# Performance work log

Measured on AMD Instinct MI355X. Metric: run time of the kernel, lower is better.

## Reference

```python
import jax, jax.numpy as jnp
import numpy as np

B, C, H, W, Q = 4, 64, 128, 128, 30000
HID = 256
IN_DIM = C * 9 + 4  # unfolded feat + rel_coord(2) + rel_cell(2)


def setup_inputs() -> dict:
    key = jax.random.key(0)
    ks = jax.random.split(key, 14)
    inp = jax.random.normal(ks[0], (B, 1, H, W), jnp.float32)
    coord = jax.random.uniform(ks[1], (B, Q, 2), jnp.float32, -1.0, 1.0)
    cell = jnp.full((B, Q, 2), 2.0 / 256.0, jnp.float32)  # HR cell size for 256x256 target
    conv_w = jax.random.normal(ks[2], (C, 1, 3, 3), jnp.float32) * 0.3
    conv_b = jnp.zeros((C,), jnp.float32)
    def lin(k, fi, fo):
        return jax.random.normal(k, (fi, fo), jnp.float32) * (1.0 / np.sqrt(fi))
    w1 = lin(ks[3], IN_DIM, HID); b1 = jnp.zeros((HID,), jnp.float32)
    w2 = lin(ks[4], HID, HID);    b2 = jnp.zeros((HID,), jnp.float32)
    w3 = lin(ks[5], HID, HID);    b3 = jnp.zeros((HID,), jnp.float32)
    w4 = lin(ks[6], HID, HID);    b4 = jnp.zeros((HID,), jnp.float32)
    w5 = lin(ks[7], HID, 1);      b5 = jnp.zeros((1,), jnp.float32)
    return dict(inp=inp, coord=coord, cell=cell, conv_w=conv_w, conv_b=conv_b,
                w1=w1, b1=b1, w2=w2, b2=b2, w3=w3, b3=b3, w4=w4, b4=b4, w5=w5, b5=b5)


def _mlp(x, w1, b1, w2, b2, w3, b3, w4, b4, w5, b5):
    h = jax.nn.relu(x @ w1 + b1)
    h = jax.nn.relu(h @ w2 + b2)
    h = jax.nn.relu(h @ w3 + b3)
    h = jax.nn.relu(h @ w4 + b4)
    return h @ w5 + b5


def reference(inp, coord, cell, conv_w, conv_b, w1, b1, w2, b2, w3, b3, w4, b4, w5, b5):
    # encoder: conv3x3, pad 1 (NCHW)
    feat = jax.lax.conv_general_dilated(
        inp, conv_w, window_strides=(1, 1), padding=((1, 1), (1, 1)),
        dimension_numbers=("NCHW", "OIHW", "NCHW")) + conv_b[None, :, None, None]
    # feat_unfold: F.unfold(feat, 3, padding=1).view(B, C*9, H, W)
    pad = jnp.pad(feat, ((0, 0), (0, 0), (1, 1), (1, 1)))
    patches = jnp.stack([pad[:, :, kh:kh + H, kw:kw + W]
                         for kh in range(3) for kw in range(3)], axis=2)  # (B,C,9,H,W)
    featu = patches.reshape(B, C * 9, H, W)
    featu_t = featu.transpose(0, 2, 3, 1).reshape(B, H * W, C * 9)  # (B,HW,Cu)

    rx = 1.0 / H  # 2/H/2
    ry = 1.0 / W
    eps_shift = 1e-6
    Hf = jnp.float32(H); Wf = jnp.float32(W)
    rel_cell = cell * jnp.array([H, W], jnp.float32)  # same for all branches

    preds, areas = [], []
    for vx in (-1.0, 1.0):
        for vy in (-1.0, 1.0):
            c0 = jnp.clip(coord[..., 0] + vx * rx + eps_shift, -1 + 1e-6, 1 - 1e-6)
            c1 = jnp.clip(coord[..., 1] + vy * ry + eps_shift, -1 + 1e-6, 1 - 1e-6)
            # nearest grid_sample, align_corners=False (round half-to-even = nearbyint)
            i = jnp.clip(jnp.round((c0 + 1.0) * Hf / 2.0 - 0.5), 0.0, Hf - 1.0)
            j = jnp.clip(jnp.round((c1 + 1.0) * Wf / 2.0 - 0.5), 0.0, Wf - 1.0)
            # q_coord = feat_coord sampled at same nearest index (pixel centers)
            qy = -1.0 + (2.0 * i + 1.0) / Hf
            qx = -1.0 + (2.0 * j + 1.0) / Wf
            idx = (i * Wf + j).astype(jnp.int32)  # (B,Q)
            q_feat = jnp.take_along_axis(featu_t, idx[..., None], axis=1)  # (B,Q,Cu)
            rel0 = (coord[..., 0] - qy) * Hf
            rel1 = (coord[..., 1] - qx) * Wf
            x = jnp.concatenate([q_feat, rel0[..., None], rel1[..., None], rel_cell], axis=-1)
            pred = _mlp(x.reshape(B * Q, -1), w1, b1, w2, b2, w3, b3, w4, b4, w5, b5)
            preds.append(pred.reshape(B, Q, -1))
            areas.append(jnp.abs(rel0 * rel1) + 1e-9)

    tot_area = areas[0] + areas[1] + areas[2] + areas[3]
    # local_ensemble: swap diagonally-opposite areas
    areas = [areas[3], areas[2], areas[1], areas[0]]
    ret = jnp.zeros_like(preds[0])
    for pred, area in zip(preds, areas):
        ret = ret + pred * (area / tot_area)[..., None]
    return ret  # (B, Q, 1)
```

## Files before the change

### kernel.cpp

```cpp
#include <hip/hip_runtime.h>
#include <stdint.h>


typedef unsigned short u16;
typedef __attribute__((ext_vector_type(8))) short   short8;
typedef __attribute__((ext_vector_type(8))) __bf16  bf16x8;
typedef __attribute__((ext_vector_type(4))) float   f32x4;

__device__ __forceinline__ float bf2f(u16 u) {
  union { uint32_t i; float f; } v; v.i = ((uint32_t)u) << 16; return v.f;
}
__device__ __forceinline__ u16 f2bf(float f) {
  union { float f; uint32_t i; } v; v.f = f;
  return (u16)((v.i + 0x7FFFu + ((v.i >> 16) & 1u)) >> 16);
}
__device__ __forceinline__ u16 bfbits(float f) {
  union { __bf16 h; u16 u; } c; c.h = (__bf16)f; return c.u;
}

__global__ void prep_weights(const float* __restrict__ w1, const float* __restrict__ w2,
                             const float* __restrict__ w3, const float* __restrict__ w4,
                             u16* __restrict__ w1pt, u16* __restrict__ w2t,
                             u16* __restrict__ w3t, u16* __restrict__ w4t) {
  int tid = blockIdx.x * 256 + threadIdx.x;
  const int N1 = 256 * 576;
  if (tid < N1) {
    int o = tid / 576, kk = tid - o * 576;
    int t = kk >> 6, c = kk & 63;
    w1pt[tid] = f2bf(w1[(c * 9 + t) * 256 + o]);
  } else {
    int u = tid - N1;
    if (u < 3 * 65536) {
      int layer = u >> 16, r = u & 65535;
      int o = r >> 8, k = r & 255;
      const float* src = (layer == 0) ? w2 : (layer == 1) ? w3 : w4;
      u16* dst = (layer == 0) ? w2t : (layer == 1) ? w3t : w4t;
      dst[o * 256 + k] = f2bf(src[k * 256 + o]);
    }
  }
}

__global__ void conv1_kernel(const float* __restrict__ inp, const float* __restrict__ cw,
                             const float* __restrict__ cb, u16* __restrict__ feat) {
  int tid = blockIdx.x * 256 + threadIdx.x;
  int c = tid & 63;
  int x = (tid >> 6) & 127;
  int y = (tid >> 13) & 127;
  int b = tid >> 20;
  const float* ip = inp + b * 16384;
  float s = cb[c];
  #pragma unroll
  for (int kh = 0; kh < 3; ++kh) {
    int iy = y + kh - 1;
    if (iy < 0 || iy > 127) continue;
    #pragma unroll
    for (int kw = 0; kw < 3; ++kw) {
      int ix = x + kw - 1;
      if (ix < 0 || ix > 127) continue;
      s += ip[iy * 128 + ix] * cw[c * 9 + kh * 3 + kw];
    }
  }
  feat[tid] = f2bf(s);
}

__global__ __launch_bounds__(256) void layer1_kernel(const u16* __restrict__ feat,
                                                     const u16* __restrict__ w1pt,
                                                     const float* __restrict__ b1,
                                                     u16* __restrict__ h1pre) {
  __shared__ short Al[64 * 40];
  __shared__ short Wl[256 * 40];

  int tid = threadIdx.x;
  int lane = tid & 63, wave = tid >> 6;
  int bid = blockIdx.x;
  int b = bid >> 8, rem = bid & 255;
  int y = rem >> 1, x0 = (rem & 1) << 6;

  f32x4 acc[4][4];
  #pragma unroll
  for (int i = 0; i < 4; ++i)
    #pragma unroll
    for (int j = 0; j < 4; ++j) acc[i][j] = (f32x4){0.f, 0.f, 0.f, 0.f};

  int apx = tid >> 2, acq = tid & 3;

  for (int kt = 0; kt < 18; ++kt) {
    __syncthreads();
    {
      int t = kt >> 1, cbase = (kt & 1) << 5;
      int dh = t / 3 - 1, dw = t % 3 - 1;
      int yy = y + dh;
      int xx = x0 + apx + dw;
      short8 v = {0, 0, 0, 0, 0, 0, 0, 0};
      if (yy >= 0 && yy < 128 && xx >= 0 && xx < 128)
        v = *(const short8*)(feat + (((b * 128 + yy) * 128 + xx) * 64 + cbase + acq * 8));
      *(short8*)(Al + apx * 40 + acq * 8) = v;
    }
    {
      #pragma unroll
      for (int it = 0; it < 5; ++it) {
        int ch = it * 256 + tid;
        int o = ch / 5, j = ch - o * 5;
        if (j < 4) {
          short8 v = *(const short8*)(w1pt + (o * 576 + kt * 32 + j * 8));
          *(short8*)(Wl + o * 40 + j * 8) = v;
        }
      }
    }
    __syncthreads();
    int g = lane >> 4, l15 = lane & 15;
    bf16x8 a[4];
    #pragma unroll
    for (int mf = 0; mf < 4; ++mf)
      a[mf] = *(const bf16x8*)(Al + (mf * 16 + l15) * 40 + g * 8);
    int wc0 = wave * 64;
    #pragma unroll
    for (int nf = 0; nf < 4; ++nf) {
      bf16x8 bfr = *(const bf16x8*)(Wl + (wc0 + nf * 16 + l15) * 40 + g * 8);
      #pragma unroll
      for (int mf = 0; mf < 4; ++mf)
        acc[mf][nf] = __builtin_amdgcn_mfma_f32_16x16x32_bf16(a[mf], bfr, acc[mf][nf], 0, 0, 0);
    }
  }

  int g = lane >> 4, l15 = lane & 15;
  int wc0 = wave * 64;
  #pragma unroll
  for (int nf = 0; nf < 4; ++nf) {
    int col = wc0 + nf * 16 + l15;
    float bias = b1[col];
    #pragma unroll
    for (int mf = 0; mf < 4; ++mf)
      #pragma unroll
      for (int i = 0; i < 4; ++i) {
        int px = mf * 16 + 4 * g + i;
        int pixel = y * 128 + x0 + px;
        h1pre[(((b << 14) + pixel) << 8) + col] = f2bf(acc[mf][nf][i] + bias);
      }
  }
}

__global__ __launch_bounds__(256, 2) void mlp_kernel(
    const float* __restrict__ coord, const float* __restrict__ cell,
    const u16* __restrict__ h1pre,
    const u16* __restrict__ w2t, const u16* __restrict__ w3t, const u16* __restrict__ w4t,
    const float* __restrict__ w1, const float* __restrict__ b2, const float* __restrict__ b3,
    const float* __restrict__ b4, const float* __restrict__ w5, const float* __restrict__ b5,
    float* __restrict__ out) {
  __shared__ short Xl[2][64 * 256];
  __shared__ float relv[128][4];
  __shared__ float area_l[128];
  __shared__ int   idx_l[128];
  __shared__ float predp[4][128];

  int tid = threadIdx.x;
  int lane = tid & 63, wave = tid >> 6;
  int g = lane >> 4, l15 = lane & 15;
  int wc0 = wave * 64;
  int xr = l15 & 7;
  int bid = blockIdx.x;

  int c16 = tid & 31;
  float wrr[4][8];
  {
    const float* wr = w1 + 576 * 256;
    #pragma unroll
    for (int a = 0; a < 4; ++a) {
      f32x4 u0 = *(const f32x4*)(wr + a * 256 + c16 * 8);
      f32x4 u1 = *(const f32x4*)(wr + a * 256 + c16 * 8 + 4);
      #pragma unroll
      for (int e = 0; e < 4; ++e) { wrr[a][e] = u0[e]; wrr[a][4 + e] = u1[e]; }
    }
  }

  if (tid < 128) {
    int t = tid >> 2, br = tid & 3;
    int gq = bid * 32 + t;
    int b = gq / 30000;
    float c0 = coord[gq * 2 + 0];
    float c1 = coord[gq * 2 + 1];
    float ce0 = cell[gq * 2 + 0];
    float ce1 = cell[gq * 2 + 1];
    float vx = (br & 2) ? 1.0f : -1.0f;
    float vy = (br & 1) ? 1.0f : -1.0f;
    float s0 = c0 + vx * (1.0f / 128.0f) + 1e-6f;
    float s1 = c1 + vy * (1.0f / 128.0f) + 1e-6f;
    s0 = fminf(fmaxf(s0, -1.0f + 1e-6f), 1.0f - 1e-6f);
    s1 = fminf(fmaxf(s1, -1.0f + 1e-6f), 1.0f - 1e-6f);
    float fi = rintf((s0 + 1.0f) * 64.0f - 0.5f);
    float fj = rintf((s1 + 1.0f) * 64.0f - 0.5f);
    fi = fminf(fmaxf(fi, 0.0f), 127.0f);
    fj = fminf(fmaxf(fj, 0.0f), 127.0f);
    float qy = -1.0f + (2.0f * fi + 1.0f) / 128.0f;
    float qx = -1.0f + (2.0f * fj + 1.0f) / 128.0f;
    float rel0 = (c0 - qy) * 128.0f;
    float rel1 = (c1 - qx) * 128.0f;
    idx_l[tid] = (b << 14) + (int)fi * 128 + (int)fj;
    relv[tid][0] = rel0;
    relv[tid][1] = rel1;
    relv[tid][2] = ce0 * 128.0f;
    relv[tid][3] = ce1 * 128.0f;
    area_l[tid] = fabsf(rel0 * rel1) + 1e-9f;
  }
  __syncthreads();

  {
    short8 v[16];
    #pragma unroll
    for (int it = 0; it < 8; ++it) {
      int rl = it * 8 + (tid >> 5);
      v[it]     = *(const short8*)(h1pre + ((size_t)idx_l[rl] << 8) + c16 * 8);
      v[8 + it] = *(const short8*)(h1pre + ((size_t)idx_l[64 + rl] << 8) + c16 * 8);
    }
    __builtin_amdgcn_sched_barrier(0);
    #pragma unroll
    for (int t = 0; t < 2; ++t) {
      #pragma unroll
      for (int it = 0; it < 8; ++it) {
        int rl = it * 8 + (tid >> 5);
        int row = t * 64 + rl;
        float r0 = relv[row][0], r1 = relv[row][1], r2 = relv[row][2], r3 = relv[row][3];
        short8 xo;
        #pragma unroll
        for (int e = 0; e < 8; ++e) {
          float val = bf2f((u16)v[t * 8 + it][e]) + r0 * wrr[0][e] + r1 * wrr[1][e] +
                      r2 * wrr[2][e] + r3 * wrr[3][e];
          xo[e] = (short)bfbits(fmaxf(val, 0.0f));
        }
        *(short8*)(&Xl[t][rl * 256 + ((c16 ^ (rl & 7)) * 8)]) = xo;
      }
    }
  }
  __syncthreads();

  const u16* Wgs[3] = {w2t, w3t, w4t};
  const float* Bgs[3] = {b2, b3, b4};

  #pragma unroll
  for (int layer = 0; layer < 3; ++layer) {
    const u16* Wg = Wgs[layer];
    const float* bias = Bgs[layer];

    bf16x8 breg[32];
    #pragma unroll
    for (int ks = 0; ks < 8; ++ks)
      #pragma unroll
      for (int nf = 0; nf < 4; ++nf)
        breg[ks * 4 + nf] =
            *(const bf16x8*)(Wg + (wc0 + nf * 16 + l15) * 256 + ks * 32 + g * 8);
    __builtin_amdgcn_sched_barrier(0);

    #pragma unroll
    for (int t = 0; t < 2; ++t) {
      f32x4 acc[4][4];
      #pragma unroll
      for (int mf = 0; mf < 4; ++mf)
        #pragma unroll
        for (int nf = 0; nf < 4; ++nf) acc[mf][nf] = (f32x4){0.f, 0.f, 0.f, 0.f};

      #pragma unroll
      for (int ks = 0; ks < 8; ++ks) {
        bf16x8 a[4];
        #pragma unroll
        for (int mf = 0; mf < 4; ++mf)
          a[mf] = *(const bf16x8*)(&Xl[t][(mf * 16 + l15) * 256 + (((ks * 4 + g) ^ xr) * 8)]);
        #pragma unroll
        for (int nf = 0; nf < 4; ++nf)
          #pragma unroll
          for (int mf = 0; mf < 4; ++mf)
            acc[mf][nf] = __builtin_amdgcn_mfma_f32_16x16x32_bf16(
                breg[ks * 4 + nf], a[mf], acc[mf][nf], 0, 0, 0);
      }

      __syncthreads();
      if (layer < 2) {
        #pragma unroll
        for (int nf = 0; nf < 4; ++nf) {
          int o0 = wc0 + nf * 16 + 4 * g;
          f32x4 bv = *(const f32x4*)(bias + o0);
          #pragma unroll
          for (int mf = 0; mf < 4; ++mf) {
            u16 p0 = bfbits(fmaxf(acc[mf][nf][0] + bv[0], 0.0f));
            u16 p1 = bfbits(fmaxf(acc[mf][nf][1] + bv[1], 0.0f));
            u16 p2 = bfbits(fmaxf(acc[mf][nf][2] + bv[2], 0.0f));
            u16 p3 = bfbits(fmaxf(acc[mf][nf][3] + bv[3], 0.0f));
            unsigned long long w =
                (unsigned long long)(p0 | ((uint32_t)p1 << 16)) |
                ((unsigned long long)(p2 | ((uint32_t)p3 << 16)) << 32);
            int idx = (mf * 16 + l15) * 256 + (((o0 >> 3) ^ xr) * 8) + (o0 & 7);
            *(unsigned long long*)(&Xl[t][idx]) = w;
          }
        }
      } else {
        float s[4] = {0.f, 0.f, 0.f, 0.f};
        #pragma unroll
        for (int nf = 0; nf < 4; ++nf) {
          int o0 = wc0 + nf * 16 + 4 * g;
          f32x4 bv = *(const f32x4*)(b4 + o0);
          f32x4 wv = *(const f32x4*)(w5 + o0);
          #pragma unroll
          for (int mf = 0; mf < 4; ++mf)
            #pragma unroll
            for (int i = 0; i < 4; ++i)
              s[mf] += fmaxf(acc[mf][nf][i] + bv[i], 0.0f) * wv[i];
        }
        #pragma unroll
        for (int mf = 0; mf < 4; ++mf) {
          s[mf] += __shfl_xor(s[mf], 16, 64);
          s[mf] += __shfl_xor(s[mf], 32, 64);
        }
        if (lane < 16) {
          #pragma unroll
          for (int mf = 0; mf < 4; ++mf)
            predp[wave][t * 64 + mf * 16 + lane] = s[mf];
        }
      }
    }
    __syncthreads();
  }

  if (tid < 32) {
    int gq = bid * 32 + tid;
    float pr[4], ar[4];
    #pragma unroll
    for (int br = 0; br < 4; ++br) {
      int r = tid * 4 + br;
      pr[br] = predp[0][r] + predp[1][r] + predp[2][r] + predp[3][r] + b5[0];
      ar[br] = area_l[r];
    }
    float tot = ar[0] + ar[1] + ar[2] + ar[3];
    float ret = 0.0f;
    #pragma unroll
    for (int br = 0; br < 4; ++br) ret += pr[br] * (ar[3 - br] / tot);
    out[gq] = ret;
  }
}

extern "C" void kernel_launch(void* const* d_in, const int* in_sizes, int n_in,
                              void* d_out, int out_size, void* d_ws, size_t ws_size,
                              hipStream_t stream) {
  const float* inp    = (const float*)d_in[0];
  const float* coord  = (const float*)d_in[1];
  const float* cell   = (const float*)d_in[2];
  const float* conv_w = (const float*)d_in[3];
  const float* conv_b = (const float*)d_in[4];
  const float* w1 = (const float*)d_in[5];
  const float* b1 = (const float*)d_in[6];
  const float* w2 = (const float*)d_in[7];
  const float* b2 = (const float*)d_in[8];
  const float* w3 = (const float*)d_in[9];
  const float* b3 = (const float*)d_in[10];
  const float* w4 = (const float*)d_in[11];
  const float* b4 = (const float*)d_in[12];
  const float* w5 = (const float*)d_in[13];
  const float* b5 = (const float*)d_in[14];
  float* out = (float*)d_out;

  char* ws = (char*)d_ws;
  u16* feat  = (u16*)(ws);
  u16* h1pre = (u16*)(ws + 8388608);
  u16* w1pt  = (u16*)(ws + 41943040);
  u16* w2t   = (u16*)(ws + 42237952);
  u16* w3t   = (u16*)(ws + 42369024);
  u16* w4t   = (u16*)(ws + 42500096);

  hipLaunchKernelGGL(prep_weights, dim3(1344), dim3(256), 0, stream,
                     w1, w2, w3, w4, w1pt, w2t, w3t, w4t);
  hipLaunchKernelGGL(conv1_kernel, dim3(16384), dim3(256), 0, stream,
                     inp, conv_w, conv_b, feat);
  hipLaunchKernelGGL(layer1_kernel, dim3(1024), dim3(256), 0, stream,
                     feat, w1pt, b1, h1pre);
  hipLaunchKernelGGL(mlp_kernel, dim3(3750), dim3(256), 0, stream,
                     coord, cell, h1pre, w2t, w3t, w4t, w1, b2, b3, b4, w5, b5, out);
}
```

Baseline: 380.8 us.

## Fold conv3x3 into first MLP layer weights to shrink K from 576 to 96

The 1-channel conv encoder is linear, so its weights and bias are pre-multiplied into the first-layer weights, giving a 90-wide (padded to 96) composed weight over raw input pixels plus a boundary-mask term. The separate conv kernel and the 576-deep layer-1 GEMM are replaced by a single kernel that builds the small patch matrix directly from the input image and runs a 3-step MFMA loop with weights held in registers. This removes the feature-map write and read and most of the layer-1 MACs. The trade-off is a different rounding path, since bf16 is now applied to composed weights and raw pixels instead of to conv features, plus a vectorised bias load and a packed 8-byte store for the output.

```diff
diff --git a/kernel.cpp b/kernel.cpp
--- a/kernel.cpp
+++ b/kernel.cpp
@@ -20,16 +20,24 @@
 
 __global__ void prep_weights(const float* __restrict__ w1, const float* __restrict__ w2,
                              const float* __restrict__ w3, const float* __restrict__ w4,
-                             u16* __restrict__ w1pt, u16* __restrict__ w2t,
+                             const float* __restrict__ cw, const float* __restrict__ cb,
+                             u16* __restrict__ W2t, u16* __restrict__ w2t,
                              u16* __restrict__ w3t, u16* __restrict__ w4t) {
   int tid = blockIdx.x * 256 + threadIdx.x;
-  const int N1 = 256 * 576;
-  if (tid < N1) {
-    int o = tid / 576, kk = tid - o * 576;
-    int t = kk >> 6, c = kk & 63;
-    w1pt[tid] = f2bf(w1[(c * 9 + t) * 256 + o]);
+  if (tid < 24576) {
+    int o = tid / 96, k = tid - o * 96;
+    float s = 0.0f;
+    if (k < 90) {
+      int t = k / 10, j = k - t * 10;
+      if (j == 9) {
+        for (int c = 0; c < 64; ++c) s += cb[c] * w1[(c * 9 + t) * 256 + o];
+      } else {
+        for (int c = 0; c < 64; ++c) s += cw[c * 9 + j] * w1[(c * 9 + t) * 256 + o];
+      }
+    }
+    W2t[o * 96 + k] = f2bf(s);
   } else {
-    int u = tid - N1;
+    int u = tid - 24576;
     if (u < 3 * 65536) {
       int layer = u >> 16, r = u & 65535;
       int o = r >> 8, k = r & 255;
@@ -40,103 +48,95 @@
   }
 }
 
-__global__ void conv1_kernel(const float* __restrict__ inp, const float* __restrict__ cw,
-                             const float* __restrict__ cb, u16* __restrict__ feat) {
-  int tid = blockIdx.x * 256 + threadIdx.x;
-  int c = tid & 63;
-  int x = (tid >> 6) & 127;
-  int y = (tid >> 13) & 127;
-  int b = tid >> 20;
-  const float* ip = inp + b * 16384;
-  float s = cb[c];
-  #pragma unroll
-  for (int kh = 0; kh < 3; ++kh) {
-    int iy = y + kh - 1;
-    if (iy < 0 || iy > 127) continue;
-    #pragma unroll
-    for (int kw = 0; kw < 3; ++kw) {
-      int ix = x + kw - 1;
-      if (ix < 0 || ix > 127) continue;
-      s += ip[iy * 128 + ix] * cw[c * 9 + kh * 3 + kw];
-    }
-  }
-  feat[tid] = f2bf(s);
-}
-
-__global__ __launch_bounds__(256) void layer1_kernel(const u16* __restrict__ feat,
-                                                     const u16* __restrict__ w1pt,
-                                                     const float* __restrict__ b1,
-                                                     u16* __restrict__ h1pre) {
-  __shared__ short Al[64 * 40];
-  __shared__ short Wl[256 * 40];
+__global__ __launch_bounds__(256) void h1pre_kernel(const float* __restrict__ inp,
+                                                    const u16* __restrict__ W2t,
+                                                    const float* __restrict__ b1,
+                                                    u16* __restrict__ h1pre) {
+  __shared__ short Al[64 * 120];
 
   int tid = threadIdx.x;
   int lane = tid & 63, wave = tid >> 6;
+  int g = lane >> 4, l15 = lane & 15;
+  int wc0 = wave * 64;
   int bid = blockIdx.x;
   int b = bid >> 8, rem = bid & 255;
   int y = rem >> 1, x0 = (rem & 1) << 6;
 
+  {
+    int px = tid >> 2, q = tid & 3;
+    int x = x0 + px;
+    const float* ip = inp + b * 16384;
+    #pragma unroll
+    for (int c8 = 0; c8 < 3; ++c8) {
+      short8 av;
+      #pragma unroll
+      for (int e = 0; e < 8; ++e) {
+        int k = q * 24 + c8 * 8 + e;
+        float val = 0.0f;
+        if (k < 90) {
+          int t = k / 10, j = k - t * 10;
+          int dh = t / 3 - 1, dw = t % 3 - 1;
+          int yy = y + dh, xx = x + dw;
+          bool m = (yy >= 0) && (yy < 128) && (xx >= 0) && (xx < 128);
+          if (j == 9) {
+            val = m ? 1.0f : 0.0f;
+          } else {
+            int sh = j / 3 - 1, sw = j % 3 - 1;
+            int r = yy + sh, c = xx + sw;
+            val = (m && r >= 0 && r < 128 && c >= 0 && c < 128) ? ip[r * 128 + c] : 0.0f;
+          }
+        }
+        av[e] = (short)f2bf(val);
+      }
+      *(short8*)(&Al[px * 120 + q * 24 + c8 * 8]) = av;
+    }
+  }
+  __syncthreads();
+
+  bf16x8 breg[12];
+  #pragma unroll
+  for (int ks = 0; ks < 3; ++ks)
+    #pragma unroll
+    for (int nf = 0; nf < 4; ++nf)
+      breg[ks * 4 + nf] =
+          *(const bf16x8*)(W2t + (wc0 + nf * 16 + l15) * 96 + ks * 32 + g * 8);
+
   f32x4 acc[4][4];
   #pragma unroll
-  for (int i = 0; i < 4; ++i)
-    #pragma unroll
-    for (int j = 0; j < 4; ++j) acc[i][j] = (f32x4){0.f, 0.f, 0.f, 0.f};
-
-  int apx = tid >> 2, acq = tid & 3;
-
-  for (int kt = 0; kt < 18; ++kt) {
-    __syncthreads();
-    {
-      int t = kt >> 1, cbase = (kt & 1) << 5;
-      int dh = t / 3 - 1, dw = t % 3 - 1;
-      int yy = y + dh;
-      int xx = x0 + apx + dw;
-      short8 v = {0, 0, 0, 0, 0, 0, 0, 0};
-      if (yy >= 0 && yy < 128 && xx >= 0 && xx < 128)
-        v = *(const short8*)(feat + (((b * 128 + yy) * 128 + xx) * 64 + cbase + acq * 8));
-      *(short8*)(Al + apx * 40 + acq * 8) = v;
-    }
-    {
-      #pragma unroll
-      for (int it = 0; it < 5; ++it) {
-        int ch = it * 256 + tid;
-        int o = ch / 5, j = ch - o * 5;
-        if (j < 4) {
-          short8 v = *(const short8*)(w1pt + (o * 576 + kt * 32 + j * 8));
-          *(short8*)(Wl + o * 40 + j * 8) = v;
-        }
-      }
-    }
-    __syncthreads();
-    int g = lane >> 4, l15 = lane & 15;
+  for (int mf = 0; mf < 4; ++mf)
+    #pragma unroll
+    for (int nf = 0; nf < 4; ++nf) acc[mf][nf] = (f32x4){0.f, 0.f, 0.f, 0.f};
+
+  #pragma unroll
+  for (int ks = 0; ks < 3; ++ks) {
     bf16x8 a[4];
     #pragma unroll
     for (int mf = 0; mf < 4; ++mf)
-      a[mf] = *(const bf16x8*)(Al + (mf * 16 + l15) * 40 + g * 8);
-    int wc0 = wave * 64;
-    #pragma unroll
-    for (int nf = 0; nf < 4; ++nf) {
-      bf16x8 bfr = *(const bf16x8*)(Wl + (wc0 + nf * 16 + l15) * 40 + g * 8);
+      a[mf] = *(const bf16x8*)(&Al[(mf * 16 + l15) * 120 + ks * 32 + g * 8]);
+    #pragma unroll
+    for (int nf = 0; nf < 4; ++nf)
       #pragma unroll
       for (int mf = 0; mf < 4; ++mf)
-        acc[mf][nf] = __builtin_amdgcn_mfma_f32_16x16x32_bf16(a[mf], bfr, acc[mf][nf], 0, 0, 0);
-    }
-  }
-
-  int g = lane >> 4, l15 = lane & 15;
-  int wc0 = wave * 64;
+        acc[mf][nf] = __builtin_amdgcn_mfma_f32_16x16x32_bf16(
+            breg[ks * 4 + nf], a[mf], acc[mf][nf], 0, 0, 0);
+  }
+
   #pragma unroll
   for (int nf = 0; nf < 4; ++nf) {
-    int col = wc0 + nf * 16 + l15;
-    float bias = b1[col];
-    #pragma unroll
-    for (int mf = 0; mf < 4; ++mf)
-      #pragma unroll
-      for (int i = 0; i < 4; ++i) {
-        int px = mf * 16 + 4 * g + i;
-        int pixel = y * 128 + x0 + px;
-        h1pre[(((b << 14) + pixel) << 8) + col] = f2bf(acc[mf][nf][i] + bias);
-      }
+    int o0 = wc0 + nf * 16 + 4 * g;
+    f32x4 bv = *(const f32x4*)(b1 + o0);
+    #pragma unroll
+    for (int mf = 0; mf < 4; ++mf) {
+      int pixel = y * 128 + x0 + mf * 16 + l15;
+      u16 p0 = f2bf(acc[mf][nf][0] + bv[0]);
+      u16 p1 = f2bf(acc[mf][nf][1] + bv[1]);
+      u16 p2 = f2bf(acc[mf][nf][2] + bv[2]);
+      u16 p3 = f2bf(acc[mf][nf][3] + bv[3]);
+      unsigned long long w =
+          (unsigned long long)(p0 | ((uint32_t)p1 << 16)) |
+          ((unsigned long long)(p2 | ((uint32_t)p3 << 16)) << 32);
+      *(unsigned long long*)(h1pre + (((size_t)((b << 14) + pixel)) << 8) + o0) = w;
+    }
   }
 }
 
@@ -357,19 +357,16 @@
   float* out = (float*)d_out;
 
   char* ws = (char*)d_ws;
-  u16* feat  = (u16*)(ws);
-  u16* h1pre = (u16*)(ws + 8388608);
-  u16* w1pt  = (u16*)(ws + 41943040);
-  u16* w2t   = (u16*)(ws + 42237952);
-  u16* w3t   = (u16*)(ws + 42369024);
-  u16* w4t   = (u16*)(ws + 42500096);
-
-  hipLaunchKernelGGL(prep_weights, dim3(1344), dim3(256), 0, stream,
-                     w1, w2, w3, w4, w1pt, w2t, w3t, w4t);
-  hipLaunchKernelGGL(conv1_kernel, dim3(16384), dim3(256), 0, stream,
-                     inp, conv_w, conv_b, feat);
-  hipLaunchKernelGGL(layer1_kernel, dim3(1024), dim3(256), 0, stream,
-                     feat, w1pt, b1, h1pre);
+  u16* h1pre = (u16*)(ws);
+  u16* W2t   = (u16*)(ws + 33554432);
+  u16* w2t   = (u16*)(ws + 33603584);
+  u16* w3t   = (u16*)(ws + 33734656);
+  u16* w4t   = (u16*)(ws + 33865728);
+
+  hipLaunchKernelGGL(prep_weights, dim3(864), dim3(256), 0, stream,
+                     w1, w2, w3, w4, conv_w, conv_b, W2t, w2t, w3t, w4t);
+  hipLaunchKernelGGL(h1pre_kernel, dim3(1024), dim3(256), 0, stream,
+                     inp, W2t, b1, h1pre);
   hipLaunchKernelGGL(mlp_kernel, dim3(3750), dim3(256), 0, stream,
                      coord, cell, h1pre, w2t, w3t, w4t, w1, b2, b3, b4, w5, b5, out);
 }
```

Measured after the change: 310.7 us (median of 2 runs). 1.23x faster.
